# Kernel tuning notes

Measured on AMD Instinct MI355X. Metric: run time of the kernel, lower is better.

## Reference

```python
import jax, jax.numpy as jnp
import numpy as np

EMBED_DIM = 256
NUM_HEADS = 8
HEAD_DIM = EMBED_DIM // NUM_HEADS
SCALE = HEAD_DIM ** (-0.5)
L, B = 2048, 2


def setup_inputs() -> dict:
    key = jax.random.key(0)
    ks = jax.random.split(key, 12)
    s = EMBED_DIM ** (-0.5)
    return {
        "query": jax.random.normal(ks[0], (L, B, EMBED_DIM), jnp.float32),
        "key_": jax.random.normal(ks[1], (L, B, EMBED_DIM), jnp.float32),
        "value": jax.random.normal(ks[2], (L, B, EMBED_DIM), jnp.float32),
        "Wq": jax.random.normal(ks[3], (EMBED_DIM, EMBED_DIM), jnp.float32) * s,
        "bq": jnp.zeros((EMBED_DIM,), jnp.float32),
        "Wk": jax.random.normal(ks[4], (EMBED_DIM, EMBED_DIM), jnp.float32) * s,
        "bk": jnp.zeros((EMBED_DIM,), jnp.float32),
        "Wv": jax.random.normal(ks[5], (EMBED_DIM, EMBED_DIM), jnp.float32) * s,
        "bv": jnp.zeros((EMBED_DIM,), jnp.float32),
        "Wp": jax.random.normal(ks[6], (EMBED_DIM, EMBED_DIM), jnp.float32) * s,
        "bp": jnp.zeros((EMBED_DIM,), jnp.float32),
    }


def reference(query, key_, value, Wq, bq, Wk, bk, Wv, bv, Wp, bp):
    # Inputs are seq-first: [L, B, E]. Dropout treated as eval (identity).
    Lq, Bq, E = query.shape
    q = (query @ Wq + bq).reshape(Lq, Bq, NUM_HEADS, HEAD_DIM)
    k = (key_ @ Wk + bk).reshape(key_.shape[0], Bq, NUM_HEADS, HEAD_DIM)
    v = (value @ Wv + bv).reshape(value.shape[0], Bq, NUM_HEADS, HEAD_DIM)
    # scores: [B, H, Lq, Lk]
    attn = jnp.einsum('qbhd,kbhd->bhqk', q, k) * SCALE
    attn = jax.nn.softmax(attn, axis=-1)
    out = jnp.einsum('bhqk,kbhd->qbhd', attn, v).reshape(Lq, Bq, E)
    return out @ Wp + bp
```

## Files before the change

### kernel.cpp

```cpp
#include <hip/hip_runtime.h>
#include <math.h>

#define L_SEQ 2048
#define BATCH 2
#define EMB   256
#define NH    8
#define HD    32
#define NROW  (L_SEQ * BATCH)
#define SCALE 0.17677669529663687f

typedef __attribute__((ext_vector_type(8))) short          short8;
typedef __attribute__((ext_vector_type(8))) unsigned short ushort8v;
typedef __attribute__((ext_vector_type(4))) unsigned short ushort4v;
typedef __attribute__((ext_vector_type(4))) float          floatx4;

__device__ __forceinline__ unsigned short f2b(float x) {
    unsigned int u = __float_as_uint(x);
    unsigned int r = u + 0x7FFFu + ((u >> 16) & 1u);
    return (unsigned short)(r >> 16);
}

__device__ __forceinline__ unsigned int pack2bf(float lo, float hi) {
    unsigned int ulo = __float_as_uint(lo);
    unsigned int uhi = __float_as_uint(hi);
    ulo += 0x7FFFu + ((ulo >> 16) & 1u);
    uhi += 0x7FFFu + ((uhi >> 16) & 1u);
    return __builtin_amdgcn_perm(uhi, ulo, 0x07060302);
}

__global__ __launch_bounds__(256) void wtrans_kernel(const float* __restrict__ Wq,
                                                     const float* __restrict__ Wk,
                                                     const float* __restrict__ Wv,
                                                     const float* __restrict__ Wp,
                                                     unsigned short* __restrict__ out) {
    __shared__ unsigned short T[64][65];
    const int wsel = blockIdx.z;
    const float* W = (wsel == 0) ? Wq : (wsel == 1) ? Wk : (wsel == 2) ? Wv : Wp;
    const float scale = (wsel == 0) ? SCALE : 1.0f;
    unsigned short* dst = out + (size_t)wsel * EMB * EMB;
    const int k0 = blockIdx.x * 64, n0 = blockIdx.y * 64;
    const int tid = threadIdx.x;

    #pragma unroll
    for (int i = 0; i < 4; ++i) {
        int idx = tid + 256 * i;
        int r = idx >> 4, c4 = (idx & 15) * 4;
        float4 f = *(const float4*)&W[(size_t)(k0 + r) * EMB + n0 + c4];
        T[r][c4 + 0] = f2b(f.x * scale);
        T[r][c4 + 1] = f2b(f.y * scale);
        T[r][c4 + 2] = f2b(f.z * scale);
        T[r][c4 + 3] = f2b(f.w * scale);
    }
    __syncthreads();
    #pragma unroll
    for (int i = 0; i < 4; ++i) {
        int idx = tid + 256 * i;
        int rn = idx >> 4, ck = (idx & 15) * 4;
        ushort4v p;
        #pragma unroll
        for (int j = 0; j < 4; ++j) p[j] = T[ck + j][rn];
        *(ushort4v*)&dst[(size_t)(n0 + rn) * EMB + k0 + ck] = p;
    }
}

__global__ __launch_bounds__(256) void qkv_proj(const float* __restrict__ Xq,
                                                const float* __restrict__ Xk,
                                                const float* __restrict__ Xv,
                                                const unsigned short* __restrict__ Wt,
                                                const float* __restrict__ bq,
                                                const float* __restrict__ bk,
                                                const float* __restrict__ bv,
                                                unsigned short* __restrict__ outq,
                                                unsigned short* __restrict__ outk,
                                                unsigned short* __restrict__ outvt) {
    __shared__ unsigned short Xs[64][264];
    __shared__ unsigned short Ws[64][264];
    const int z = blockIdx.z;
    const float* X    = (z == 0) ? Xq : (z == 1) ? Xk : Xv;
    const float* bias = (z == 0) ? bq : (z == 1) ? bk : bv;
    const float bscale = (z == 0) ? SCALE : 1.0f;
    const unsigned short* W = Wt + (size_t)z * EMB * EMB;

    const int row0 = blockIdx.x * 64;
    const int col0 = blockIdx.y * 64;
    const int tid  = threadIdx.x;
    const int w    = tid >> 6;
    const int lane = tid & 63;
    const int l16  = lane & 15;
    const int quad = lane >> 4;

    #pragma unroll
    for (int i = 0; i < 8; ++i) {
        int idx = tid + 256 * i;
        int r = idx >> 5, c8 = (idx & 31) * 8;
        const float4* xp = (const float4*)&X[(size_t)(row0 + r) * EMB + c8];
        float4 f0 = xp[0], f1 = xp[1];
        uint4 pk;
        pk.x = pack2bf(f0.x, f0.y); pk.y = pack2bf(f0.z, f0.w);
        pk.z = pack2bf(f1.x, f1.y); pk.w = pack2bf(f1.z, f1.w);
        *(uint4*)&Xs[r][c8] = pk;
        *(ushort8v*)&Ws[r][c8] = *(const ushort8v*)&W[(size_t)(col0 + r) * EMB + c8];
    }
    __syncthreads();

    floatx4 acc[4];
    #pragma unroll
    for (int g = 0; g < 4; ++g) acc[g] = (floatx4){0.f, 0.f, 0.f, 0.f};

    #pragma unroll
    for (int k = 0; k < EMB; k += 32) {
        short8 a = *(const short8*)&Xs[w * 16 + l16][k + quad * 8];
        #pragma unroll
        for (int g = 0; g < 4; ++g) {
            short8 bf = *(const short8*)&Ws[g * 16 + l16][k + quad * 8];
            acc[g] = __builtin_amdgcn_mfma_f32_16x16x32_bf16(a, bf, acc[g], 0, 0, 0);
        }
    }

    if (z == 2) {
        __syncthreads();
        #pragma unroll
        for (int g = 0; g < 4; ++g) {
            int n = g * 16 + l16;
            float bb = bias[col0 + n] * bscale;
            #pragma unroll
            for (int r = 0; r < 4; ++r)
                Xs[w * 16 + quad * 4 + r][n] = f2b(acc[g][r] + bb);
        }
        __syncthreads();
        #pragma unroll
        for (int i = 0; i < 2; ++i) {
            int idx = tid + 256 * i;
            int n = idx >> 3, sub = idx & 7;
            int bb2 = sub >> 2, lq = sub & 3;
            ushort8v p;
            #pragma unroll
            for (int j = 0; j < 8; ++j) p[j] = Xs[(lq * 8 + j) * 2 + bb2][n];
            int h = (col0 + n) >> 5, d = (col0 + n) & 31;
            size_t base = ((size_t)(bb2 * NH + h) * HD + d) * L_SEQ + (row0 >> 1) + lq * 8;
            *(ushort8v*)&outvt[base] = p;
        }
    } else {
        unsigned short* outp = z ? outk : outq;
        #pragma unroll
        for (int g = 0; g < 4; ++g) {
            int c = col0 + g * 16 + l16;
            float bb = bias[c] * bscale;
            #pragma unroll
            for (int r = 0; r < 4; ++r) {
                int rg = row0 + w * 16 + quad * 4 + r;
                int b = rg & 1, ll = rg >> 1;
                int h = c >> 5, d = c & 31;
                outp[(((size_t)(b * NH + h) * L_SEQ) + ll) * HD + d] = f2b(acc[g][r] + bb);
            }
        }
    }
}

__global__ __launch_bounds__(256) void out_proj(const unsigned short* __restrict__ X,
                                                const unsigned short* __restrict__ Wt,
                                                const float* __restrict__ bias,
                                                float* __restrict__ out) {
    __shared__ unsigned short Xs[64][264];
    __shared__ unsigned short Ws[64][264];
    const int row0 = blockIdx.x * 64;
    const int col0 = blockIdx.y * 64;
    const int tid  = threadIdx.x;
    const int w    = tid >> 6;
    const int lane = tid & 63;
    const int l16  = lane & 15;
    const int quad = lane >> 4;

    #pragma unroll
    for (int i = 0; i < 8; ++i) {
        int idx = tid + 256 * i;
        int r = idx >> 5, c8 = (idx & 31) * 8;
        *(ushort8v*)&Xs[r][c8] = *(const ushort8v*)&X[(size_t)(row0 + r) * EMB + c8];
        *(ushort8v*)&Ws[r][c8] = *(const ushort8v*)&Wt[(size_t)(col0 + r) * EMB + c8];
    }
    __syncthreads();

    floatx4 acc[4];
    #pragma unroll
    for (int g = 0; g < 4; ++g) acc[g] = (floatx4){0.f, 0.f, 0.f, 0.f};

    #pragma unroll
    for (int k = 0; k < EMB; k += 32) {
        short8 a = *(const short8*)&Xs[w * 16 + l16][k + quad * 8];
        #pragma unroll
        for (int g = 0; g < 4; ++g) {
            short8 bf = *(const short8*)&Ws[g * 16 + l16][k + quad * 8];
            acc[g] = __builtin_amdgcn_mfma_f32_16x16x32_bf16(a, bf, acc[g], 0, 0, 0);
        }
    }

    #pragma unroll
    for (int g = 0; g < 4; ++g) {
        int c = col0 + g * 16 + l16;
        float bb = bias[c];
        #pragma unroll
        for (int r = 0; r < 4; ++r) {
            int rg = row0 + w * 16 + quad * 4 + r;
            out[(size_t)rg * EMB + c] = acc[g][r] + bb;
        }
    }
}

__global__ __launch_bounds__(256) void attn_kernel(const unsigned short* __restrict__ Q,
                                                   const unsigned short* __restrict__ K,
                                                   const unsigned short* __restrict__ Vt,
                                                   unsigned short* __restrict__ ctx) {
    __shared__ unsigned short Vs[2][32][72];
    __shared__ unsigned short Ps[4][16][72];

    const int tid  = threadIdx.x;
    const int w    = tid >> 6;
    const int lane = tid & 63;
    const int l16  = lane & 15;
    const int quad = lane >> 4;

    const int l0 = blockIdx.x * 64;
    const int h  = blockIdx.y;
    const int b  = blockIdx.z;
    const size_t bh = (size_t)(b * NH + h);

    const unsigned short* Qg  = Q  + (bh * L_SEQ) * HD;
    const unsigned short* Kg  = K  + (bh * L_SEQ) * HD;
    const unsigned short* Vtg = Vt + (bh * HD) * L_SEQ;

    short8 qfrag = *(const short8*)&Qg[(size_t)(l0 + w * 16 + l16) * HD + quad * 8];

    float m = -INFINITY, l = 0.0f;
    floatx4 o0 = {0.f, 0.f, 0.f, 0.f};
    floatx4 o1 = {0.f, 0.f, 0.f, 0.f};
    const floatx4 zero4 = {0.f, 0.f, 0.f, 0.f};

    const int vd = tid >> 3;
    const int vj = (tid & 7) * 8;

    *(ushort8v*)&Vs[0][vd][vj] = *(const ushort8v*)&Vtg[(size_t)vd * L_SEQ + vj];

    const int NT = L_SEQ / 64;
    for (int kt = 0; kt < NT; ++kt) {
        __syncthreads();

        ushort8v vnext;
        if (kt + 1 < NT)
            vnext = *(const ushort8v*)&Vtg[(size_t)vd * L_SEQ + (kt + 1) * 64 + vj];

        floatx4 s[4];
        #pragma unroll
        for (int g = 0; g < 4; ++g) {
            short8 kfrag = *(const short8*)
                &Kg[(size_t)(kt * 64 + g * 16 + l16) * HD + quad * 8];
            s[g] = __builtin_amdgcn_mfma_f32_16x16x32_bf16(kfrag, qfrag, zero4, 0, 0, 0);
        }

        float mx = s[0][0];
        #pragma unroll
        for (int g = 0; g < 4; ++g)
            #pragma unroll
            for (int r = 0; r < 4; ++r) mx = fmaxf(mx, s[g][r]);
        mx = fmaxf(mx, __shfl_xor(mx, 16));
        mx = fmaxf(mx, __shfl_xor(mx, 32));

        float mnew = fmaxf(m, mx);
        float al = __expf(m - mnew);
        m = mnew;

        float ls = 0.0f;
        #pragma unroll
        for (int g = 0; g < 4; ++g) {
            float p0 = __expf(s[g][0] - m);
            float p1 = __expf(s[g][1] - m);
            float p2 = __expf(s[g][2] - m);
            float p3 = __expf(s[g][3] - m);
            ls += (p0 + p1) + (p2 + p3);
            uint2 pk;
            pk.x = pack2bf(p0, p1);
            pk.y = pack2bf(p2, p3);
            *(uint2*)&Ps[w][l16][g * 16 + quad * 4] = pk;
        }
        ls += __shfl_xor(ls, 16);
        ls += __shfl_xor(ls, 32);
        l = al * l + ls;

        #pragma unroll
        for (int r = 0; r < 4; ++r) { o0[r] *= al; o1[r] *= al; }

        const unsigned short (*Vc)[72] = Vs[kt & 1];
        short8 pf0 = *(const short8*)&Ps[w][l16][quad * 8];
        short8 pf1 = *(const short8*)&Ps[w][l16][32 + quad * 8];
        short8 v00 = *(const short8*)&Vc[l16][quad * 8];
        short8 v01 = *(const short8*)&Vc[16 + l16][quad * 8];
        short8 v10 = *(const short8*)&Vc[l16][32 + quad * 8];
        short8 v11 = *(const short8*)&Vc[16 + l16][32 + quad * 8];

        o0 = __builtin_amdgcn_mfma_f32_16x16x32_bf16(v00, pf0, o0, 0, 0, 0);
        o0 = __builtin_amdgcn_mfma_f32_16x16x32_bf16(v10, pf1, o0, 0, 0, 0);
        o1 = __builtin_amdgcn_mfma_f32_16x16x32_bf16(v01, pf0, o1, 0, 0, 0);
        o1 = __builtin_amdgcn_mfma_f32_16x16x32_bf16(v11, pf1, o1, 0, 0, 0);

        if (kt + 1 < NT)
            *(ushort8v*)&Vs[(kt + 1) & 1][vd][vj] = vnext;
    }

    float invl = 1.0f / l;
    int query = l0 + w * 16 + l16;
    size_t base = ((size_t)query * BATCH + b) * EMB + h * HD;
    uint2 e0, e1;
    e0.x = pack2bf(o0[0] * invl, o0[1] * invl);
    e0.y = pack2bf(o0[2] * invl, o0[3] * invl);
    e1.x = pack2bf(o1[0] * invl, o1[1] * invl);
    e1.y = pack2bf(o1[2] * invl, o1[3] * invl);
    *(uint2*)&ctx[base + quad * 4] = e0;
    *(uint2*)&ctx[base + 16 + quad * 4] = e1;
}

extern "C" void kernel_launch(void* const* d_in, const int* in_sizes, int n_in,
                              void* d_out, int out_size, void* d_ws, size_t ws_size,
                              hipStream_t stream) {
    const float* query = (const float*)d_in[0];
    const float* key_  = (const float*)d_in[1];
    const float* value = (const float*)d_in[2];
    const float* Wq    = (const float*)d_in[3];
    const float* bq    = (const float*)d_in[4];
    const float* Wk    = (const float*)d_in[5];
    const float* bk    = (const float*)d_in[6];
    const float* Wv    = (const float*)d_in[7];
    const float* bv    = (const float*)d_in[8];
    const float* Wp    = (const float*)d_in[9];
    const float* bp    = (const float*)d_in[10];
    float* out = (float*)d_out;

    unsigned short* ws = (unsigned short*)d_ws;
    const size_t WSZ = (size_t)EMB * EMB;
    const size_t M   = (size_t)NROW * EMB;
    unsigned short* wt  = ws;
    unsigned short* qw  = ws + 4 * WSZ;
    unsigned short* kw  = qw + M;
    unsigned short* vtw = kw + M;
    unsigned short* ctx = vtw + M;

    wtrans_kernel<<<dim3(4, 4, 4), 256, 0, stream>>>(Wq, Wk, Wv, Wp, wt);

    qkv_proj<<<dim3(NROW / 64, EMB / 64, 3), 256, 0, stream>>>(
        query, key_, value, wt, bq, bk, bv, qw, kw, vtw);

    attn_kernel<<<dim3(L_SEQ / 64, NH, BATCH), 256, 0, stream>>>(qw, kw, vtw, ctx);

    out_proj<<<dim3(NROW / 64, EMB / 64), 256, 0, stream>>>(ctx, wt + 3 * WSZ, bp, out);
}
```

Before: 129.4 us.

## Widen attention key tile to 128, prefetch K into registers, shrink out_proj tiles

The attention kernel now handles 128 keys per iteration instead of 64, which halves the number of online-softmax rescales and barriers. It also loads the next tile's K fragments into registers while the current tile is computed, so global K loads overlap with MFMA work. Separately, out_proj uses 32x32 output tiles with one 16x16 tile per wave, which launches more blocks to fill the GPU. In exchange, register and LDS use per attention block rise, which may lower occupancy.

```diff
diff --git a/kernel.cpp b/kernel.cpp
--- a/kernel.cpp
+++ b/kernel.cpp
@@ -161,64 +161,57 @@
                                                 const unsigned short* __restrict__ Wt,
                                                 const float* __restrict__ bias,
                                                 float* __restrict__ out) {
-    __shared__ unsigned short Xs[64][264];
-    __shared__ unsigned short Ws[64][264];
-    const int row0 = blockIdx.x * 64;
-    const int col0 = blockIdx.y * 64;
+    __shared__ unsigned short Xs[32][264];
+    __shared__ unsigned short Ws[32][264];
+    const int row0 = blockIdx.x * 32;
+    const int col0 = blockIdx.y * 32;
+    const int tid  = threadIdx.x;
+    const int w    = tid >> 6;
+    const int rw   = (w & 1) * 16;
+    const int cw   = (w >> 1) * 16;
+    const int lane = tid & 63;
+    const int l16  = lane & 15;
+    const int quad = lane >> 4;
+
+    #pragma unroll
+    for (int i = 0; i < 4; ++i) {
+        int idx = tid + 256 * i;
+        int r = idx >> 5, c8 = (idx & 31) * 8;
+        *(ushort8v*)&Xs[r][c8] = *(const ushort8v*)&X[(size_t)(row0 + r) * EMB + c8];
+        *(ushort8v*)&Ws[r][c8] = *(const ushort8v*)&Wt[(size_t)(col0 + r) * EMB + c8];
+    }
+    __syncthreads();
+
+    floatx4 acc = {0.f, 0.f, 0.f, 0.f};
+    #pragma unroll
+    for (int k = 0; k < EMB; k += 32) {
+        short8 a  = *(const short8*)&Xs[rw + l16][k + quad * 8];
+        short8 bf = *(const short8*)&Ws[cw + l16][k + quad * 8];
+        acc = __builtin_amdgcn_mfma_f32_16x16x32_bf16(a, bf, acc, 0, 0, 0);
+    }
+
+    int c = col0 + cw + l16;
+    float bb = bias[c];
+    #pragma unroll
+    for (int r = 0; r < 4; ++r) {
+        int rg = row0 + rw + quad * 4 + r;
+        out[(size_t)rg * EMB + c] = acc[r] + bb;
+    }
+}
+
+__global__ __launch_bounds__(256) void attn_kernel(const unsigned short* __restrict__ Q,
+                                                   const unsigned short* __restrict__ K,
+                                                   const unsigned short* __restrict__ Vt,
+                                                   unsigned short* __restrict__ ctx) {
+    __shared__ unsigned short Vs[2][32][136];
+    __shared__ unsigned short Ps[4][16][136];
+
     const int tid  = threadIdx.x;
     const int w    = tid >> 6;
     const int lane = tid & 63;
     const int l16  = lane & 15;
     const int quad = lane >> 4;
 
-    #pragma unroll
-    for (int i = 0; i < 8; ++i) {
-        int idx = tid + 256 * i;
-        int r = idx >> 5, c8 = (idx & 31) * 8;
-        *(ushort8v*)&Xs[r][c8] = *(const ushort8v*)&X[(size_t)(row0 + r) * EMB + c8];
-        *(ushort8v*)&Ws[r][c8] = *(const ushort8v*)&Wt[(size_t)(col0 + r) * EMB + c8];
-    }
-    __syncthreads();
-
-    floatx4 acc[4];
-    #pragma unroll
-    for (int g = 0; g < 4; ++g) acc[g] = (floatx4){0.f, 0.f, 0.f, 0.f};
-
-    #pragma unroll
-    for (int k = 0; k < EMB; k += 32) {
-        short8 a = *(const short8*)&Xs[w * 16 + l16][k + quad * 8];
-        #pragma unroll
-        for (int g = 0; g < 4; ++g) {
-            short8 bf = *(const short8*)&Ws[g * 16 + l16][k + quad * 8];
-            acc[g] = __builtin_amdgcn_mfma_f32_16x16x32_bf16(a, bf, acc[g], 0, 0, 0);
-        }
-    }
-
-    #pragma unroll
-    for (int g = 0; g < 4; ++g) {
-        int c = col0 + g * 16 + l16;
-        float bb = bias[c];
-        #pragma unroll
-        for (int r = 0; r < 4; ++r) {
-            int rg = row0 + w * 16 + quad * 4 + r;
-            out[(size_t)rg * EMB + c] = acc[g][r] + bb;
-        }
-    }
-}
-
-__global__ __launch_bounds__(256) void attn_kernel(const unsigned short* __restrict__ Q,
-                                                   const unsigned short* __restrict__ K,
-                                                   const unsigned short* __restrict__ Vt,
-                                                   unsigned short* __restrict__ ctx) {
-    __shared__ unsigned short Vs[2][32][72];
-    __shared__ unsigned short Ps[4][16][72];
-
-    const int tid  = threadIdx.x;
-    const int w    = tid >> 6;
-    const int lane = tid & 63;
-    const int l16  = lane & 15;
-    const int quad = lane >> 4;
-
     const int l0 = blockIdx.x * 64;
     const int h  = blockIdx.y;
     const int b  = blockIdx.z;
@@ -238,27 +231,36 @@
     const int vd = tid >> 3;
     const int vj = (tid & 7) * 8;
 
-    *(ushort8v*)&Vs[0][vd][vj] = *(const ushort8v*)&Vtg[(size_t)vd * L_SEQ + vj];
-
-    const int NT = L_SEQ / 64;
+    short8 kf[8];
+    #pragma unroll
+    for (int g = 0; g < 8; ++g)
+        kf[g] = *(const short8*)&Kg[(size_t)(g * 16 + l16) * HD + quad * 8];
+
+    *(ushort8v*)&Vs[0][vd][vj]      = *(const ushort8v*)&Vtg[(size_t)vd * L_SEQ + vj];
+    *(ushort8v*)&Vs[0][vd][64 + vj] = *(const ushort8v*)&Vtg[(size_t)vd * L_SEQ + 64 + vj];
+
+    const int NT = L_SEQ / 128;
     for (int kt = 0; kt < NT; ++kt) {
         __syncthreads();
 
-        ushort8v vnext;
-        if (kt + 1 < NT)
-            vnext = *(const ushort8v*)&Vtg[(size_t)vd * L_SEQ + (kt + 1) * 64 + vj];
-
-        floatx4 s[4];
-        #pragma unroll
-        for (int g = 0; g < 4; ++g) {
-            short8 kfrag = *(const short8*)
-                &Kg[(size_t)(kt * 64 + g * 16 + l16) * HD + quad * 8];
-            s[g] = __builtin_amdgcn_mfma_f32_16x16x32_bf16(kfrag, qfrag, zero4, 0, 0, 0);
+        floatx4 s[8];
+        #pragma unroll
+        for (int g = 0; g < 8; ++g)
+            s[g] = __builtin_amdgcn_mfma_f32_16x16x32_bf16(kf[g], qfrag, zero4, 0, 0, 0);
+
+        ushort8v vn0, vn1;
+        if (kt + 1 < NT) {
+            #pragma unroll
+            for (int g = 0; g < 8; ++g)
+                kf[g] = *(const short8*)
+                    &Kg[(size_t)((kt + 1) * 128 + g * 16 + l16) * HD + quad * 8];
+            vn0 = *(const ushort8v*)&Vtg[(size_t)vd * L_SEQ + (kt + 1) * 128 + vj];
+            vn1 = *(const ushort8v*)&Vtg[(size_t)vd * L_SEQ + (kt + 1) * 128 + 64 + vj];
         }
 
         float mx = s[0][0];
         #pragma unroll
-        for (int g = 0; g < 4; ++g)
+        for (int g = 0; g < 8; ++g)
             #pragma unroll
             for (int r = 0; r < 4; ++r) mx = fmaxf(mx, s[g][r]);
         mx = fmaxf(mx, __shfl_xor(mx, 16));
@@ -270,7 +272,7 @@
 
         float ls = 0.0f;
         #pragma unroll
-        for (int g = 0; g < 4; ++g) {
+        for (int g = 0; g < 8; ++g) {
             float p0 = __expf(s[g][0] - m);
             float p1 = __expf(s[g][1] - m);
             float p2 = __expf(s[g][2] - m);
@@ -288,21 +290,20 @@
         #pragma unroll
         for (int r = 0; r < 4; ++r) { o0[r] *= al; o1[r] *= al; }
 
-        const unsigned short (*Vc)[72] = Vs[kt & 1];
-        short8 pf0 = *(const short8*)&Ps[w][l16][quad * 8];
-        short8 pf1 = *(const short8*)&Ps[w][l16][32 + quad * 8];
-        short8 v00 = *(const short8*)&Vc[l16][quad * 8];
-        short8 v01 = *(const short8*)&Vc[16 + l16][quad * 8];
-        short8 v10 = *(const short8*)&Vc[l16][32 + quad * 8];
-        short8 v11 = *(const short8*)&Vc[16 + l16][32 + quad * 8];
-
-        o0 = __builtin_amdgcn_mfma_f32_16x16x32_bf16(v00, pf0, o0, 0, 0, 0);
-        o0 = __builtin_amdgcn_mfma_f32_16x16x32_bf16(v10, pf1, o0, 0, 0, 0);
-        o1 = __builtin_amdgcn_mfma_f32_16x16x32_bf16(v01, pf0, o1, 0, 0, 0);
-        o1 = __builtin_amdgcn_mfma_f32_16x16x32_bf16(v11, pf1, o1, 0, 0, 0);
-
-        if (kt + 1 < NT)
-            *(ushort8v*)&Vs[(kt + 1) & 1][vd][vj] = vnext;
+        const unsigned short (*Vc)[136] = Vs[kt & 1];
+        #pragma unroll
+        for (int c = 0; c < 4; ++c) {
+            short8 pf = *(const short8*)&Ps[w][l16][c * 32 + quad * 8];
+            short8 va = *(const short8*)&Vc[l16][c * 32 + quad * 8];
+            short8 vb = *(const short8*)&Vc[16 + l16][c * 32 + quad * 8];
+            o0 = __builtin_amdgcn_mfma_f32_16x16x32_bf16(va, pf, o0, 0, 0, 0);
+            o1 = __builtin_amdgcn_mfma_f32_16x16x32_bf16(vb, pf, o1, 0, 0, 0);
+        }
+
+        if (kt + 1 < NT) {
+            *(ushort8v*)&Vs[(kt + 1) & 1][vd][vj]      = vn0;
+            *(ushort8v*)&Vs[(kt + 1) & 1][vd][64 + vj] = vn1;
+        }
     }
 
     float invl = 1.0f / l;
@@ -349,5 +350,5 @@
 
     attn_kernel<<<dim3(L_SEQ / 64, NH, BATCH), 256, 0, stream>>>(qw, kw, vtw, ctx);
 
-    out_proj<<<dim3(NROW / 64, EMB / 64), 256, 0, stream>>>(ctx, wt + 3 * WSZ, bp, out);
-}
+    out_proj<<<dim3(NROW / 32, EMB / 32), 256, 0, stream>>>(ctx, wt + 3 * WSZ, bp, out);
+}
```

New measurement: 122.9 us. 1.05x faster.
